# Optimization experiments

Measured on AMD Instinct MI355X. Metric: run time of the kernel, lower is better.

Reference implementation:

```python
import jax, jax.numpy as jnp
import numpy as np

VOCAB, EMBED, HIDDEN = 32000, 512, 1024
BATCH, SEQ = 32, 48
PAD = 0


def setup_inputs() -> dict:
    key = jax.random.key(0)
    ks = jax.random.split(key, 10)
    s = 0.02
    emb = jax.random.normal(ks[0], (VOCAB, EMBED), jnp.float32) * s
    emb = emb.at[PAD].set(0.0)  # padding_idx row zeroed
    return {
        "inputs": jax.random.randint(ks[1], (BATCH, SEQ), 0, VOCAB),
        "hidden": jax.random.normal(ks[2], (BATCH, HIDDEN), jnp.float32),
        "cell": jax.random.normal(ks[3], (BATCH, HIDDEN), jnp.float32),
        "emb": emb,
        "W_ih": jax.random.normal(ks[4], (4 * HIDDEN, EMBED), jnp.float32) * s,
        "W_hh": jax.random.normal(ks[5], (4 * HIDDEN, HIDDEN), jnp.float32) * s,
        "b_ih": jnp.zeros((4 * HIDDEN,), jnp.float32),
        "b_hh": jnp.zeros((4 * HIDDEN,), jnp.float32),
        "fc_W": jax.random.normal(ks[6], (VOCAB, HIDDEN), jnp.float32) * s,
        "fc_b": jnp.zeros((VOCAB,), jnp.float32),
        "generate_len": 50,
    }


def reference(inputs, hidden, cell, emb, W_ih, W_hh, b_ih, b_hh, fc_W, fc_b, generate_len):
    # Training-path forward (dropout treated as identity for determinism).
    x = emb[inputs]                      # [B, S, E]
    xs = jnp.transpose(x, (1, 0, 2))     # [S, B, E] time-major

    def step(carry, x_t):
        h, c = carry
        gates = x_t @ W_ih.T + b_ih + h @ W_hh.T + b_hh  # [B, 4H]
        i, f, g, o = jnp.split(gates, 4, axis=-1)
        c_new = jax.nn.sigmoid(f) * c + jax.nn.sigmoid(i) * jnp.tanh(g)
        h_new = jax.nn.sigmoid(o) * jnp.tanh(c_new)
        logits = h_new @ fc_W.T + fc_b                   # [B, V]
        return (h_new, c_new), logits

    _, out = jax.lax.scan(step, (hidden, cell), xs)      # [S, B, V]
    return jnp.transpose(out, (1, 0, 2))                 # [B, S, V]
```

## Files before the change

### kernel.cpp

```cpp
#include <hip/hip_runtime.h>
#include <stdint.h>


typedef unsigned short u16;
typedef __attribute__((ext_vector_type(8))) short bf16x8;
typedef __attribute__((ext_vector_type(4))) float floatx4;
struct alignas(8) us4 { u16 x, y, z, w; };

#define BATCH 32
#define SEQ   48
#define EMBED 512
#define HID   1024
#define VOCAB 32000
#define MROWS (SEQ * BATCH)

__device__ __forceinline__ u16 f2bf(float f) {
  unsigned u = __float_as_uint(f);
  u += 0x7FFF + ((u >> 16) & 1);
  return (u16)(u >> 16);
}

__device__ __forceinline__ floatx4 mfma16(bf16x8 a, bf16x8 b, floatx4 c) {
  return __builtin_amdgcn_mfma_f32_16x16x32_bf16(a, b, c, 0, 0, 0);
}

typedef __attribute__((address_space(1))) unsigned int as1_uint;
typedef __attribute__((address_space(3))) unsigned int as3_uint;
__device__ __forceinline__ void gl_lds16(const void* g, void* l) {
  __builtin_amdgcn_global_load_lds((as1_uint*)g, (as3_uint*)l, 16, 0, 0);
}

__device__ __forceinline__ float sigmoidf_(float x) {
  return 1.0f / (1.0f + __expf(-x));
}

__global__ void cast_kernel(const float* __restrict__ in, u16* __restrict__ out, int n4) {
  int i = blockIdx.x * blockDim.x + threadIdx.x;
  if (i < n4) {
    float4 v = *(const float4*)(in + (size_t)i * 4);
    us4 o;
    o.x = f2bf(v.x); o.y = f2bf(v.y); o.z = f2bf(v.z); o.w = f2bf(v.w);
    *(us4*)(out + (size_t)i * 4) = o;
  }
}

__global__ void gather_kernel(const int* __restrict__ idx, const float* __restrict__ emb,
                              u16* __restrict__ X) {
  int bid = blockIdx.x;
  int s = bid >> 5, b = bid & 31;
  int t = idx[b * SEQ + s];
  const float* src = emb + (size_t)t * EMBED;
  u16* dst = X + (size_t)bid * EMBED;
  int e = threadIdx.x * 4;
  float4 v = *(const float4*)(src + e);
  us4 o;
  o.x = f2bf(v.x); o.y = f2bf(v.y); o.z = f2bf(v.z); o.w = f2bf(v.w);
  *(us4*)(dst + e) = o;
}

__global__ __launch_bounds__(256) void gemm_bt_kernel(
    const u16* __restrict__ A, const u16* __restrict__ B,
    const float* __restrict__ bias0, const float* __restrict__ bias1,
    float* __restrict__ C, int M, int N, int K, int out_mode) {
  __shared__ u16 As[128 * 64];
  __shared__ u16 Bs[128 * 64];

  const int tid = threadIdx.x;
  const int wave = tid >> 6, lane = tid & 63;
  const int l3 = lane >> 3, l7 = lane & 7;
  const int q = lane >> 4, rf = lane & 15;
  const int tn = blockIdx.x, tm = blockIdx.y;
  const int gm0 = tm * 128, gn0 = tn * 128;
  const int wm = (wave & 1) * 64, wn = (wave >> 1) * 64;

  floatx4 acc[4][4];
#pragma unroll
  for (int i = 0; i < 4; ++i)
#pragma unroll
    for (int j = 0; j < 4; ++j) acc[i][j] = (floatx4){0.f, 0.f, 0.f, 0.f};

  for (int k0 = 0; k0 < K; k0 += 64) {
#pragma unroll
    for (int i = 0; i < 4; ++i) {
      int e = wave * 4 + i;
      int r = e * 8 + l3;
      int qd = l7 ^ (r & 7);
      gl_lds16(A + (size_t)(gm0 + r) * K + k0 + qd * 8, (void*)(As + e * 512));
      gl_lds16(B + (size_t)(gn0 + r) * K + k0 + qd * 8, (void*)(Bs + e * 512));
    }
    __syncthreads();

#pragma unroll
    for (int kk = 0; kk < 64; kk += 32) {
      int jc = (kk >> 3) + q;
      bf16x8 af[4], bf[4];
#pragma unroll
      for (int mi = 0; mi < 4; ++mi) {
        int r = wm + mi * 16 + rf;
        af[mi] = *(const bf16x8*)(As + r * 64 + (jc ^ (r & 7)) * 8);
      }
#pragma unroll
      for (int ni = 0; ni < 4; ++ni) {
        int r = wn + ni * 16 + rf;
        bf[ni] = *(const bf16x8*)(Bs + r * 64 + (jc ^ (r & 7)) * 8);
      }
#pragma unroll
      for (int mi = 0; mi < 4; ++mi)
#pragma unroll
        for (int ni = 0; ni < 4; ++ni)
          acc[mi][ni] = mfma16(af[mi], bf[ni], acc[mi][ni]);
    }
    __syncthreads();
  }

#pragma unroll
  for (int ni = 0; ni < 4; ++ni) {
    int n = gn0 + wn + ni * 16 + rf;
    float bv = bias0[n];
    if (bias1) bv += bias1[n];
#pragma unroll
    for (int mi = 0; mi < 4; ++mi) {
#pragma unroll
      for (int r = 0; r < 4; ++r) {
        int m = gm0 + wm + mi * 16 + q * 4 + r;
        float val = acc[mi][ni][r] + bv;
        if (out_mode == 0) {
          C[(size_t)m * N + n] = val;
        } else {
          int b = m & 31, s = m >> 5;
          C[((size_t)b * SEQ + s) * N + n] = val;
        }
      }
    }
  }
}

__global__ __launch_bounds__(256) void lstm_step_kernel(
    const u16* __restrict__ h_prev,
    const u16* __restrict__ Whh,
    const float* __restrict__ xg,
    const float* __restrict__ c_in,
    float* __restrict__ c_out,
    u16* __restrict__ h_out) {
  const int u0 = blockIdx.x * 4;
  const int tid = threadIdx.x;
  const int wave = tid >> 6, lane = tid & 63;
  const int q = lane >> 4, rf = lane & 15;
  const int gate = rf >> 2, du = rf & 3;
  const int brow = gate * HID + u0 + du;

  floatx4 acc0 = {0.f, 0.f, 0.f, 0.f}, acc1 = {0.f, 0.f, 0.f, 0.f};
  const u16* wp = Whh + (size_t)brow * HID + wave * 256 + q * 8;
  const u16* a0p = h_prev + (size_t)rf * HID + wave * 256 + q * 8;
  const u16* a1p = a0p + 16 * HID;
#pragma unroll
  for (int ks = 0; ks < 256; ks += 32) {
    bf16x8 bv = *(const bf16x8*)(wp + ks);
    bf16x8 a0 = *(const bf16x8*)(a0p + ks);
    bf16x8 a1 = *(const bf16x8*)(a1p + ks);
    acc0 = mfma16(a0, bv, acc0);
    acc1 = mfma16(a1, bv, acc1);
  }

  __shared__ float red[4][32][16];
#pragma unroll
  for (int r = 0; r < 4; ++r) {
    red[wave][q * 4 + r][rf] = acc0[r];
    red[wave][16 + q * 4 + r][rf] = acc1[r];
  }
  __syncthreads();

  if (tid < 128) {
    int b = tid >> 2, d = tid & 3;
    int u = u0 + d;
    float g4[4];
#pragma unroll
    for (int gt = 0; gt < 4; ++gt) {
      int n = gt * 4 + d;
      float v = red[0][b][n] + red[1][b][n] + red[2][b][n] + red[3][b][n];
      v += xg[b * 4096 + gt * HID + u];
      g4[gt] = v;
    }
    float i_ = sigmoidf_(g4[0]);
    float f_ = sigmoidf_(g4[1]);
    float gg = tanhf(g4[2]);
    float o_ = sigmoidf_(g4[3]);
    float c = f_ * c_in[b * HID + u] + i_ * gg;
    float h = o_ * tanhf(c);
    c_out[b * HID + u] = c;
    h_out[b * HID + u] = f2bf(h);
  }
}

extern "C" void kernel_launch(void* const* d_in, const int* in_sizes, int n_in,
                              void* d_out, int out_size, void* d_ws, size_t ws_size,
                              hipStream_t stream) {
  const int*   inputs = (const int*)d_in[0];
  const float* hidden = (const float*)d_in[1];
  const float* cell   = (const float*)d_in[2];
  const float* emb    = (const float*)d_in[3];
  const float* W_ih   = (const float*)d_in[4];
  const float* W_hh   = (const float*)d_in[5];
  const float* b_ih   = (const float*)d_in[6];
  const float* b_hh   = (const float*)d_in[7];
  const float* fc_W   = (const float*)d_in[8];
  const float* fc_b   = (const float*)d_in[9];
  float* out = (float*)d_out;

  char* ws = (char*)d_ws;
  u16*   Xbf  = (u16*)(ws);
  u16*   Wihb = (u16*)(ws + 1572864);
  u16*   Whhb = (u16*)(ws + 1572864 + 4194304);
  u16*   fcWb = (u16*)(ws + 14155776);
  float* Xg   = (float*)(ws + 14155776 + 65536000);
  u16*   Hall = (u16*)(ws + 104857600);
  float* c_ws = (float*)(ws + 104857600 + 3211264);

  cast_kernel<<<(4096 * 512 / 4 + 255) / 256, 256, 0, stream>>>(W_ih, Wihb, 4096 * 512 / 4);
  cast_kernel<<<(4096 * 1024 / 4 + 255) / 256, 256, 0, stream>>>(W_hh, Whhb, 4096 * 1024 / 4);
  cast_kernel<<<(VOCAB * 1024 / 4 + 255) / 256, 256, 0, stream>>>(fc_W, fcWb, VOCAB * 1024 / 4);
  cast_kernel<<<(BATCH * HID / 4 + 255) / 256, 256, 0, stream>>>(hidden, Hall, BATCH * HID / 4);

  gather_kernel<<<MROWS, 128, 0, stream>>>(inputs, emb, Xbf);

  gemm_bt_kernel<<<dim3(4096 / 128, MROWS / 128), 256, 0, stream>>>(
      Xbf, Wihb, b_ih, b_hh, Xg, MROWS, 4096, EMBED, 0);

  for (int s = 0; s < SEQ; ++s) {
    lstm_step_kernel<<<256, 256, 0, stream>>>(
        Hall + (size_t)s * BATCH * HID, Whhb, Xg + (size_t)s * BATCH * 4096,
        (s == 0) ? cell : c_ws, c_ws, Hall + (size_t)(s + 1) * BATCH * HID);
  }

  gemm_bt_kernel<<<dim3(VOCAB / 128, MROWS / 128), 256, 0, stream>>>(
      Hall + (size_t)BATCH * HID, fcWb, fc_b, (const float*)nullptr, out,
      MROWS, VOCAB, HID, 1);
}
```

Baseline: 819.4 us.

## Fuse LSTM recurrence into persistent cooperative kernel and remap GEMM tiles per XCD

Replaces the 48 per-timestep LSTM kernel launches with one cooperative persistent kernel. It keeps the cell state in registers and uses grid.sync between steps. If the cooperative launch fails, it falls back to the old per-step launches. Separately, GEMM workgroup IDs are remapped so that consecutive tiles are grouped per chiplet (XCD) and M tiles iterate fastest, which is meant to improve L2 reuse of the weight tiles. The cost is grid-wide barrier overhead and the requirement that all 256 blocks be co-resident.

```diff
diff --git a/kernel.cpp b/kernel.cpp
--- a/kernel.cpp
+++ b/kernel.cpp
@@ -1,5 +1,8 @@
 #include <hip/hip_runtime.h>
+#include <hip/hip_cooperative_groups.h>
 #include <stdint.h>
+
+namespace cg = cooperative_groups;
 
 
 typedef unsigned short u16;
@@ -69,7 +72,19 @@
   const int wave = tid >> 6, lane = tid & 63;
   const int l3 = lane >> 3, l7 = lane & 7;
   const int q = lane >> 4, rf = lane & 15;
-  const int tn = blockIdx.x, tm = blockIdx.y;
+
+  const int mt = gridDim.y;
+  const int nwg = gridDim.x * mt;
+  int lid = blockIdx.y * gridDim.x + blockIdx.x;
+  int work;
+  if ((nwg & 7) == 0) {
+    int per = nwg >> 3;
+    work = (lid & 7) * per + (lid >> 3);
+  } else {
+    work = lid;
+  }
+  const int tn = work / mt, tm = work % mt;
+
   const int gm0 = tm * 128, gn0 = tn * 128;
   const int wm = (wave & 1) * 64, wn = (wave >> 1) * 64;
 
@@ -189,6 +204,72 @@
     float h = o_ * tanhf(c);
     c_out[b * HID + u] = c;
     h_out[b * HID + u] = f2bf(h);
+  }
+}
+
+__global__ __launch_bounds__(256, 1) void lstm_persist_kernel(
+    const u16* __restrict__ Whh,
+    const float* __restrict__ xg_all,
+    const float* __restrict__ c_init,
+    u16* __restrict__ Hall) {
+  cg::grid_group grid = cg::this_grid();
+
+  const int u0 = blockIdx.x * 4;
+  const int tid = threadIdx.x;
+  const int wave = tid >> 6, lane = tid & 63;
+  const int q = lane >> 4, rf = lane & 15;
+  const int gate = rf >> 2, du = rf & 3;
+  const int brow = gate * HID + u0 + du;
+
+  __shared__ float red[4][32][16];
+
+  const int ab = tid >> 2, ad = tid & 3;
+  float c_reg = 0.f;
+  if (tid < 128) c_reg = c_init[ab * HID + u0 + ad];
+
+  const u16* wp = Whh + (size_t)brow * HID + wave * 256 + q * 8;
+
+  for (int s = 0; s < SEQ; ++s) {
+    const u16* h_prev = Hall + (size_t)s * BATCH * HID;
+    const float* xg = xg_all + (size_t)s * BATCH * 4096;
+    const u16* a0p = h_prev + (size_t)rf * HID + wave * 256 + q * 8;
+    const u16* a1p = a0p + 16 * HID;
+
+    floatx4 acc0 = {0.f, 0.f, 0.f, 0.f}, acc1 = {0.f, 0.f, 0.f, 0.f};
+#pragma unroll
+    for (int ks = 0; ks < 256; ks += 32) {
+      bf16x8 bv = *(const bf16x8*)(wp + ks);
+      bf16x8 a0 = *(const bf16x8*)(a0p + ks);
+      bf16x8 a1 = *(const bf16x8*)(a1p + ks);
+      acc0 = mfma16(a0, bv, acc0);
+      acc1 = mfma16(a1, bv, acc1);
+    }
+
+#pragma unroll
+    for (int r = 0; r < 4; ++r) {
+      red[wave][q * 4 + r][rf] = acc0[r];
+      red[wave][16 + q * 4 + r][rf] = acc1[r];
+    }
+    __syncthreads();
+
+    if (tid < 128) {
+      float g4[4];
+#pragma unroll
+      for (int gt = 0; gt < 4; ++gt) {
+        int n = gt * 4 + ad;
+        float v = red[0][ab][n] + red[1][ab][n] + red[2][ab][n] + red[3][ab][n];
+        v += xg[ab * 4096 + gt * HID + u0 + ad];
+        g4[gt] = v;
+      }
+      float i_ = sigmoidf_(g4[0]);
+      float f_ = sigmoidf_(g4[1]);
+      float gg = tanhf(g4[2]);
+      float o_ = sigmoidf_(g4[3]);
+      c_reg = f_ * c_reg + i_ * gg;
+      float h = o_ * tanhf(c_reg);
+      Hall[(size_t)(s + 1) * BATCH * HID + ab * HID + u0 + ad] = f2bf(h);
+    }
+    grid.sync();
   }
 }
 
@@ -226,10 +307,22 @@
   gemm_bt_kernel<<<dim3(4096 / 128, MROWS / 128), 256, 0, stream>>>(
       Xbf, Wihb, b_ih, b_hh, Xg, MROWS, 4096, EMBED, 0);
 
-  for (int s = 0; s < SEQ; ++s) {
-    lstm_step_kernel<<<256, 256, 0, stream>>>(
-        Hall + (size_t)s * BATCH * HID, Whhb, Xg + (size_t)s * BATCH * 4096,
-        (s == 0) ? cell : c_ws, c_ws, Hall + (size_t)(s + 1) * BATCH * HID);
+  {
+    const u16*   whh_p  = Whhb;
+    const float* xg_p   = Xg;
+    const float* c_p    = cell;
+    u16*         hall_p = Hall;
+    void* kargs[] = {(void*)&whh_p, (void*)&xg_p, (void*)&c_p, (void*)&hall_p};
+    hipError_t cerr = hipLaunchCooperativeKernel(
+        reinterpret_cast<const void*>(&lstm_persist_kernel),
+        dim3(256), dim3(256), kargs, 0, stream);
+    if (cerr != hipSuccess) {
+      for (int s = 0; s < SEQ; ++s) {
+        lstm_step_kernel<<<256, 256, 0, stream>>>(
+            Hall + (size_t)s * BATCH * HID, Whhb, Xg + (size_t)s * BATCH * 4096,
+            (s == 0) ? cell : c_ws, c_ws, Hall + (size_t)(s + 1) * BATCH * HID);
+      }
+    }
   }
 
   gemm_bt_kernel<<<dim3(VOCAB / 128, MROWS / 128), 256, 0, stream>>>(
```

New measurement: 2.108 ms. 2.57x slower.

## Fuse LSTM recurrence into one persistent kernel with global atomic barrier

Applied to the files above, without the earlier changes.

Replaces the 48 per-timestep launches with a single persistent kernel of 256 blocks. The blocks synchronise each step through an atomic counter in global memory, and the cell state stays in registers. h is read with cache-bypassing loads and written with packed atomic stores. The GEMM also remaps block IDs so tiles are grouped across XCDs. The change removes launch overhead and c round-trips, but it depends on all 256 blocks being co-resident and on the spin barrier being correct.

```diff
diff --git a/kernel.cpp b/kernel.cpp
--- a/kernel.cpp
+++ b/kernel.cpp
@@ -32,6 +32,13 @@
 
 __device__ __forceinline__ float sigmoidf_(float x) {
   return 1.0f / (1.0f + __expf(-x));
+}
+
+__device__ __forceinline__ void ld_c16(bf16x8& d, const u16* p) {
+  asm volatile("global_load_dwordx4 %0, %1, off sc0 sc1" : "=&v"(d) : "v"(p));
+}
+__device__ __forceinline__ void ld_n16(bf16x8& d, const u16* p) {
+  asm volatile("global_load_dwordx4 %0, %1, off" : "=&v"(d) : "v"(p));
 }
 
 __global__ void cast_kernel(const float* __restrict__ in, u16* __restrict__ out, int n4) {
@@ -45,8 +52,9 @@
 }
 
 __global__ void gather_kernel(const int* __restrict__ idx, const float* __restrict__ emb,
-                              u16* __restrict__ X) {
+                              u16* __restrict__ X, unsigned* __restrict__ bar) {
   int bid = blockIdx.x;
+  if (bid == 0 && threadIdx.x == 0) *bar = 0u;
   int s = bid >> 5, b = bid & 31;
   int t = idx[b * SEQ + s];
   const float* src = emb + (size_t)t * EMBED;
@@ -69,7 +77,19 @@
   const int wave = tid >> 6, lane = tid & 63;
   const int l3 = lane >> 3, l7 = lane & 7;
   const int q = lane >> 4, rf = lane & 15;
-  const int tn = blockIdx.x, tm = blockIdx.y;
+
+  const int mt = gridDim.y;
+  const int nwg = gridDim.x * mt;
+  int lid = blockIdx.y * gridDim.x + blockIdx.x;
+  int work;
+  if ((nwg & 7) == 0) {
+    int per = nwg >> 3;
+    work = (lid & 7) * per + (lid >> 3);
+  } else {
+    work = lid;
+  }
+  const int tn = work / mt, tm = work % mt;
+
   const int gm0 = tm * 128, gn0 = tn * 128;
   const int wm = (wave & 1) * 64, wn = (wave >> 1) * 64;
 
@@ -135,13 +155,12 @@
   }
 }
 
-__global__ __launch_bounds__(256) void lstm_step_kernel(
-    const u16* __restrict__ h_prev,
+__global__ __launch_bounds__(256, 1) void lstm_persist2_kernel(
     const u16* __restrict__ Whh,
-    const float* __restrict__ xg,
-    const float* __restrict__ c_in,
-    float* __restrict__ c_out,
-    u16* __restrict__ h_out) {
+    const float* __restrict__ xg_all,
+    const float* __restrict__ c_init,
+    u16* __restrict__ Hall,
+    unsigned* __restrict__ bar) {
   const int u0 = blockIdx.x * 4;
   const int tid = threadIdx.x;
   const int wave = tid >> 6, lane = tid & 63;
@@ -149,46 +168,78 @@
   const int gate = rf >> 2, du = rf & 3;
   const int brow = gate * HID + u0 + du;
 
-  floatx4 acc0 = {0.f, 0.f, 0.f, 0.f}, acc1 = {0.f, 0.f, 0.f, 0.f};
+  __shared__ float red[4][32][16];
+
+  const int ab = tid >> 2, ad = tid & 3;
+  float c_reg = 0.f;
+  if (tid < 128) c_reg = c_init[ab * HID + u0 + ad];
+
   const u16* wp = Whh + (size_t)brow * HID + wave * 256 + q * 8;
-  const u16* a0p = h_prev + (size_t)rf * HID + wave * 256 + q * 8;
-  const u16* a1p = a0p + 16 * HID;
-#pragma unroll
-  for (int ks = 0; ks < 256; ks += 32) {
-    bf16x8 bv = *(const bf16x8*)(wp + ks);
-    bf16x8 a0 = *(const bf16x8*)(a0p + ks);
-    bf16x8 a1 = *(const bf16x8*)(a1p + ks);
-    acc0 = mfma16(a0, bv, acc0);
-    acc1 = mfma16(a1, bv, acc1);
-  }
-
-  __shared__ float red[4][32][16];
-#pragma unroll
-  for (int r = 0; r < 4; ++r) {
-    red[wave][q * 4 + r][rf] = acc0[r];
-    red[wave][16 + q * 4 + r][rf] = acc1[r];
-  }
-  __syncthreads();
-
-  if (tid < 128) {
-    int b = tid >> 2, d = tid & 3;
-    int u = u0 + d;
-    float g4[4];
-#pragma unroll
-    for (int gt = 0; gt < 4; ++gt) {
-      int n = gt * 4 + d;
-      float v = red[0][b][n] + red[1][b][n] + red[2][b][n] + red[3][b][n];
-      v += xg[b * 4096 + gt * HID + u];
-      g4[gt] = v;
-    }
-    float i_ = sigmoidf_(g4[0]);
-    float f_ = sigmoidf_(g4[1]);
-    float gg = tanhf(g4[2]);
-    float o_ = sigmoidf_(g4[3]);
-    float c = f_ * c_in[b * HID + u] + i_ * gg;
-    float h = o_ * tanhf(c);
-    c_out[b * HID + u] = c;
-    h_out[b * HID + u] = f2bf(h);
+  const unsigned nwg = gridDim.x;
+
+  for (int s = 0; s < SEQ; ++s) {
+    const u16* h_prev = Hall + (size_t)s * BATCH * HID;
+    const float* xg = xg_all + (size_t)s * BATCH * 4096;
+    const u16* a0p = h_prev + (size_t)rf * HID + wave * 256 + q * 8;
+    const u16* a1p = a0p + 16 * HID;
+
+    bf16x8 wv[8], a0v[8], a1v[8];
+#pragma unroll
+    for (int i = 0; i < 8; ++i) {
+      ld_n16(wv[i], wp + i * 32);
+      ld_c16(a0v[i], a0p + i * 32);
+      ld_c16(a1v[i], a1p + i * 32);
+    }
+    asm volatile("s_waitcnt vmcnt(0)" ::: "memory");
+    __builtin_amdgcn_sched_barrier(0);
+
+    floatx4 acc0 = {0.f, 0.f, 0.f, 0.f}, acc1 = {0.f, 0.f, 0.f, 0.f};
+#pragma unroll
+    for (int i = 0; i < 8; ++i) {
+      acc0 = mfma16(a0v[i], wv[i], acc0);
+      acc1 = mfma16(a1v[i], wv[i], acc1);
+    }
+
+#pragma unroll
+    for (int r = 0; r < 4; ++r) {
+      red[wave][q * 4 + r][rf] = acc0[r];
+      red[wave][16 + q * 4 + r][rf] = acc1[r];
+    }
+    __syncthreads();
+
+    if (tid < 128) {
+      float g4[4];
+#pragma unroll
+      for (int gt = 0; gt < 4; ++gt) {
+        int n = gt * 4 + ad;
+        float v = red[0][ab][n] + red[1][ab][n] + red[2][ab][n] + red[3][ab][n];
+        v += xg[ab * 4096 + gt * HID + u0 + ad];
+        g4[gt] = v;
+      }
+      float i_ = sigmoidf_(g4[0]);
+      float f_ = sigmoidf_(g4[1]);
+      float gg = tanhf(g4[2]);
+      float o_ = sigmoidf_(g4[3]);
+      c_reg = f_ * c_reg + i_ * gg;
+      float hv = o_ * tanhf(c_reg);
+      u16 hb = f2bf(hv);
+      float hn = __shfl_xor(hv, 1);
+      u16 nb = f2bf(hn);
+      if ((tid & 1) == 0) {
+        unsigned w = (unsigned)hb | ((unsigned)nb << 16);
+        unsigned* dst = (unsigned*)(Hall + (size_t)(s + 1) * BATCH * HID +
+                                    ab * HID + u0 + ad);
+        __hip_atomic_store(dst, w, __ATOMIC_RELAXED, __HIP_MEMORY_SCOPE_AGENT);
+      }
+    }
+    __syncthreads();
+    if (tid == 0) {
+      __hip_atomic_fetch_add(bar, 1u, __ATOMIC_RELAXED, __HIP_MEMORY_SCOPE_AGENT);
+      unsigned target = nwg * (unsigned)(s + 1);
+      while (__hip_atomic_load(bar, __ATOMIC_RELAXED, __HIP_MEMORY_SCOPE_AGENT) < target)
+        __builtin_amdgcn_s_sleep(2);
+    }
+    __syncthreads();
   }
 }
 
@@ -214,23 +265,19 @@
   u16*   fcWb = (u16*)(ws + 14155776);
   float* Xg   = (float*)(ws + 14155776 + 65536000);
   u16*   Hall = (u16*)(ws + 104857600);
-  float* c_ws = (float*)(ws + 104857600 + 3211264);
+  unsigned* bar = (unsigned*)(ws + 104857600 + 3211264);
 
   cast_kernel<<<(4096 * 512 / 4 + 255) / 256, 256, 0, stream>>>(W_ih, Wihb, 4096 * 512 / 4);
   cast_kernel<<<(4096 * 1024 / 4 + 255) / 256, 256, 0, stream>>>(W_hh, Whhb, 4096 * 1024 / 4);
   cast_kernel<<<(VOCAB * 1024 / 4 + 255) / 256, 256, 0, stream>>>(fc_W, fcWb, VOCAB * 1024 / 4);
   cast_kernel<<<(BATCH * HID / 4 + 255) / 256, 256, 0, stream>>>(hidden, Hall, BATCH * HID / 4);
 
-  gather_kernel<<<MROWS, 128, 0, stream>>>(inputs, emb, Xbf);
+  gather_kernel<<<MROWS, 128, 0, stream>>>(inputs, emb, Xbf, bar);
 
   gemm_bt_kernel<<<dim3(4096 / 128, MROWS / 128), 256, 0, stream>>>(
       Xbf, Wihb, b_ih, b_hh, Xg, MROWS, 4096, EMBED, 0);
 
-  for (int s = 0; s < SEQ; ++s) {
-    lstm_step_kernel<<<256, 256, 0, stream>>>(
-        Hall + (size_t)s * BATCH * HID, Whhb, Xg + (size_t)s * BATCH * 4096,
-        (s == 0) ? cell : c_ws, c_ws, Hall + (size_t)(s + 1) * BATCH * HID);
-  }
+  lstm_persist2_kernel<<<256, 256, 0, stream>>>(Whhb, Xg, cell, Hall, bar);
 
   gemm_bt_kernel<<<dim3(VOCAB / 128, MROWS / 128), 256, 0, stream>>>(
       Hall + (size_t)BATCH * HID, fcWb, fc_b, (const float*)nullptr, out,
```

Measured after the change: 981.0 us. +19.7%, slower.
